# Optimization experiments

Measured on AMD Instinct MI355X. Metric: run time of the kernel, lower is better.

Reference implementation:

```python
import jax, jax.numpy as jnp
import numpy as np
import math

DIM = 2048
H = 16
KV = 4
HD = DIM // H  # 128
ROPE_DIM = 64  # head_dim * rope_fraction(0.5), even
ROPE_BASE = 10000.0
EPS_RMS = 1.1920928955078125e-07  # torch fp32 finfo eps (F.rms_norm default)


def rms_norm(t):
    # F.rms_norm over last dim, no weight
    return t * jax.lax.rsqrt(jnp.mean(t * t, axis=-1, keepdims=True) + EPS_RMS)


def rope_tables(seqlen, dtype):
    inv_freq = 1.0 / (ROPE_BASE ** (jnp.arange(0, ROPE_DIM, 2, dtype=jnp.float32) / ROPE_DIM))
    t = jnp.arange(seqlen, dtype=jnp.float32)
    freqs = jnp.outer(t, inv_freq)  # [S, ROPE_DIM//2]
    return jnp.cos(freqs).astype(dtype)[None, None], jnp.sin(freqs).astype(dtype)[None, None]


def apply_partial_rope(x, cos, sin):
    # x: [B, h, S, HD]; rotate first ROPE_DIM dims, pass through the rest
    xr = x[..., :ROPE_DIM]
    half = ROPE_DIM // 2
    x1, x2 = xr[..., :half], xr[..., half:]
    rotated = jnp.concatenate((x1 * cos + x2 * sin, -x1 * sin + x2 * cos), axis=-1)
    return jnp.concatenate((rotated, x[..., ROPE_DIM:]), axis=-1)


def setup_inputs() -> dict:
    key = jax.random.key(0)
    ks = jax.random.split(key, 5)
    B, S = 4, 1024
    x = jax.random.normal(ks[0], (B, S, DIM), dtype=jnp.float32)
    Wq = jax.random.normal(ks[1], (DIM, DIM), dtype=jnp.float32) * 0.02
    Wk = jax.random.normal(ks[2], (KV * HD, DIM), dtype=jnp.float32) * 0.02
    Wv = jax.random.normal(ks[3], (KV * HD, DIM), dtype=jnp.float32) * 0.02
    Wproj = jax.random.normal(ks[4], (DIM, DIM), dtype=jnp.float32) * 0.02
    # causal boolean mask [B, S, S]
    causal = jnp.tril(jnp.ones((S, S), dtype=bool))
    attn_mask = jnp.broadcast_to(causal[None], (B, S, S))
    return {"x": x, "attn_mask": attn_mask, "Wq": Wq, "Wk": Wk, "Wv": Wv, "Wproj": Wproj}


def reference(x, attn_mask, Wq, Wk, Wv, Wproj):
    B, S, D = x.shape
    repeat = H // KV
    q = (x @ Wq.T).reshape(B, S, H, HD).transpose(0, 2, 1, 3)   # [B,H,S,HD]
    k = (x @ Wk.T).reshape(B, S, KV, HD).transpose(0, 2, 1, 3)  # [B,KV,S,HD]
    v = (x @ Wv.T).reshape(B, S, KV, HD).transpose(0, 2, 1, 3)
    q = rms_norm(q)
    k = rms_norm(k)
    cos, sin = rope_tables(S, q.dtype)
    q = apply_partial_rope(q, cos, sin)
    k = apply_partial_rope(k, cos, sin)
    # GQA: expand kv heads
    k_rep = jnp.repeat(k, repeat, axis=1)  # [B,H,S,HD]
    v_rep = jnp.repeat(v, repeat, axis=1)
    bias = jnp.where(attn_mask[:, None], jnp.float32(0.0), jnp.float32(-10000.0)).astype(q.dtype)
    scores = jnp.einsum('bhqd,bhkd->bhqk', q, k_rep) / math.sqrt(HD) + bias
    attn = jax.nn.softmax(scores, axis=-1)
    y = jnp.einsum('bhqk,bhkd->bhqd', attn, v_rep)
    valid = jnp.any(attn_mask, axis=-1)[:, None, :, None].astype(y.dtype)
    y = y * valid
    # xsa: remove component of y along self value vector
    denom = jnp.maximum(jnp.sum(v_rep * v_rep, axis=-1, keepdims=True), 1e-06)
    proj = jnp.sum(y * v_rep, axis=-1, keepdims=True) / denom
    y = y - proj * v_rep
    y = y.transpose(0, 2, 1, 3).reshape(B, S, D)
    return y @ Wproj.T
```

## Files before the change

kernel.cpp:

```cpp
#include <hip/hip_runtime.h>


typedef __attribute__((ext_vector_type(8))) __bf16 bf16x8;
typedef __attribute__((ext_vector_type(4))) __bf16 bf16x4;
typedef __attribute__((ext_vector_type(4))) float f32x4;

static_assert(sizeof(__bf16) == 2, "bf16 size");

#define MFMA16x16x32(a, b, c) __builtin_amdgcn_mfma_f32_16x16x32_bf16((a), (b), (c), 0, 0, 0)

#if __has_builtin(__builtin_amdgcn_exp2f)
#define EXP2(x) __builtin_amdgcn_exp2f(x)
#else
#define EXP2(x) exp2f(x)
#endif

__device__ __forceinline__ void gload_lds16(const void* g, void* l) {
  __builtin_amdgcn_global_load_lds((const __attribute__((address_space(1))) void*)g,
                                   (__attribute__((address_space(3))) void*)l, 16, 0, 0);
}

__global__ __launch_bounds__(256) void prep(const float* __restrict__ x,
                                            const float* __restrict__ wq,
                                            const float* __restrict__ wk,
                                            const float* __restrict__ wv,
                                            const float* __restrict__ wp,
                                            __bf16* __restrict__ xb,
                                            __bf16* __restrict__ wb,
                                            __bf16* __restrict__ wpb,
                                            float2* __restrict__ tab) {
  constexpr int NX = 2097152;
  constexpr int NW1 = 1048576;
  constexpr int NW2 = 262144;
  constexpr int NP = 1048576;
  constexpr int NT = 32768;
  constexpr int TOT = NX + NW1 + 2 * NW2 + NP + NT;
  auto cast4 = [](const float* s, __bf16* d, int i) {
    f32x4 v = ((const f32x4*)s)[i];
    bf16x4 o;
    o[0] = (__bf16)v[0];
    o[1] = (__bf16)v[1];
    o[2] = (__bf16)v[2];
    o[3] = (__bf16)v[3];
    ((bf16x4*)d)[i] = o;
  };
  int i = blockIdx.x * blockDim.x + threadIdx.x;
  const int stride = gridDim.x * blockDim.x;
  for (; i < TOT; i += stride) {
    int j = i;
    if (j < NX) {
      cast4(x, xb, j);
    } else if ((j -= NX) < NW1) {
      cast4(wq, wb, j);
    } else if ((j -= NW1) < NW2) {
      cast4(wk, wb + (size_t)NW1 * 4, j);
    } else if ((j -= NW2) < NW2) {
      cast4(wv, wb + (size_t)(NW1 + NW2) * 4, j);
    } else if ((j -= NW2) < NP) {
      cast4(wp, wpb, j);
    } else {
      j -= NP;
      const int s = j >> 5, jj = j & 31;
      const float inv = powf(10000.0f, -(float)jj * 0.03125f);
      const float ang = (float)s * inv;
      tab[j] = make_float2(cosf(ang), sinf(ang));
    }
  }
}

template <typename CT, bool FUSE>
__global__ __launch_bounds__(256) void gemm_bt(const __bf16* __restrict__ A,
                                               const __bf16* __restrict__ B,
                                               CT* __restrict__ C, int N, int K, int nbn,
                                               const float2* __restrict__ tab) {
  __shared__ __bf16 As[3][128 * 32];
  __shared__ __bf16 Bs[3][128 * 32];
  const int nwg = gridDim.x;
  const int id = blockIdx.x;
  const int xid = (id & 7) * (nwg >> 3) + (id >> 3);
  const int bm = xid / nbn;
  const int bn = xid - bm * nbn;
  const int t = threadIdx.x;
  const int l = t & 63, w = t >> 6;
  const int wr = w >> 1, wc = w & 1;
  const int lr = l & 15, lk = l >> 4;
  const __bf16* Ab = A + (size_t)bm * 128 * K;
  const __bf16* Bb = B + (size_t)bn * 128 * K;
  const int srow = t >> 2;
  const int scol = ((t & 3) ^ ((srow >> 1) & 3)) << 3;
  f32x4 acc[4][4] = {};

  auto stage = [&](int kt, int buf) {
    const int k0 = kt << 5;
    gload_lds16(Ab + (size_t)srow * K + k0 + scol, &As[buf][t * 8]);
    gload_lds16(Ab + (size_t)(srow + 64) * K + k0 + scol, &As[buf][2048 + t * 8]);
    gload_lds16(Bb + (size_t)srow * K + k0 + scol, &Bs[buf][t * 8]);
    gload_lds16(Bb + (size_t)(srow + 64) * K + k0 + scol, &Bs[buf][2048 + t * 8]);
  };

  stage(0, 0);
  stage(1, 1);
  asm volatile("s_waitcnt vmcnt(4)" ::: "memory");
  __builtin_amdgcn_s_barrier();

  const int NT = K >> 5;
  int cur = 0;
  for (int kt = 0; kt < NT; ++kt) {
    if (kt + 2 < NT) {
      int c2 = cur + 2;
      if (c2 >= 3) c2 -= 3;
      stage(kt + 2, c2);
    }

    bf16x8 af[4], bfr[4];
#pragma unroll
    for (int m = 0; m < 4; ++m) {
      const int row = wr * 64 + m * 16 + lr;
      af[m] = *(const bf16x8*)&As[cur][row * 32 + ((lk ^ ((row >> 1) & 3)) << 3)];
    }
#pragma unroll
    for (int n = 0; n < 4; ++n) {
      const int row = wc * 64 + n * 16 + lr;
      bfr[n] = *(const bf16x8*)&Bs[cur][row * 32 + ((lk ^ ((row >> 1) & 3)) << 3)];
    }
#pragma unroll
    for (int m = 0; m < 4; ++m)
#pragma unroll
      for (int n = 0; n < 4; ++n) acc[m][n] = MFMA16x16x32(af[m], bfr[n], acc[m][n]);

    if (kt + 2 < NT)
      asm volatile("s_waitcnt vmcnt(4)" ::: "memory");
    else
      asm volatile("s_waitcnt vmcnt(0)" ::: "memory");
    __builtin_amdgcn_s_barrier();

    ++cur;
    if (cur == 3) cur = 0;
  }

  if constexpr (FUSE) {
    if (bn < 20) {
      __syncthreads();
      __shared__ float Ls[2][128];
      float ssp[4][4];
#pragma unroll
      for (int m = 0; m < 4; ++m)
#pragma unroll
        for (int i = 0; i < 4; ++i) {
          float s = 0.0f;
#pragma unroll
          for (int n = 0; n < 4; ++n) s += acc[m][n][i] * acc[m][n][i];
#pragma unroll
          for (int off = 1; off < 16; off <<= 1) s += __shfl_xor(s, off);
          ssp[m][i] = s;
        }
      if (lr == 0) {
#pragma unroll
        for (int m = 0; m < 4; ++m)
#pragma unroll
          for (int i = 0; i < 4; ++i)
            Ls[wc][wr * 64 + m * 16 + lk * 4 + i] = ssp[m][i];
      }
      __syncthreads();
      const bool isq = (bn < 16);
      const float qs = isq ? 0.1275174457f : 1.0f;
#pragma unroll
      for (int m = 0; m < 4; ++m) {
#pragma unroll
        for (int i = 0; i < 4; ++i) {
          const int rl = wr * 64 + m * 16 + lk * 4 + i;
          const int rg = bm * 128 + rl;
          const float sc =
              rsqrtf((Ls[0][rl] + Ls[1][rl]) * (1.0f / 128.0f) +
                     1.1920928955078125e-07f) *
              qs;
          CT* Cr = C + (size_t)rg * N + bn * 128;
          if (wc == 0) {
            const int s = rg & 1023;
#pragma unroll
            for (int n = 0; n < 2; ++n) {
              const int j = n * 16 + lr;
              const float2 cs = tab[s * 32 + j];
              const float x1 = acc[m][n][i], x2 = acc[m][n + 2][i];
              Cr[j] = (CT)((x1 * cs.x + x2 * cs.y) * sc);
              Cr[j + 32] = (CT)((-x1 * cs.y + x2 * cs.x) * sc);
            }
          } else {
#pragma unroll
            for (int n = 0; n < 4; ++n)
              Cr[64 + n * 16 + lr] = (CT)(acc[m][n][i] * sc);
          }
        }
      }
      return;
    }
  }

#pragma unroll
  for (int m = 0; m < 4; ++m) {
    const int row0 = bm * 128 + wr * 64 + m * 16 + lk * 4;
#pragma unroll
    for (int n = 0; n < 4; ++n) {
      const int col = bn * 128 + wc * 64 + n * 16 + lr;
#pragma unroll
      for (int i = 0; i < 4; ++i) C[(size_t)(row0 + i) * N + col] = (CT)acc[m][n][i];
    }
  }
}

__global__ __launch_bounds__(256) void vtrans(const __bf16* __restrict__ qkv,
                                              __bf16* __restrict__ vt) {
  __shared__ __bf16 L[64 * 128];
  const int tile = blockIdx.x;
  const int st = tile & 15, bk = tile >> 4;
  const int b = bk >> 2, kvh = bk & 3;
  const int t = threadIdx.x;
  const int s0 = st * 64;
  const __bf16* src = qkv + ((size_t)(b * 1024 + s0)) * 3072 + 2560 + kvh * 128;
#pragma unroll
  for (int r = 0; r < 4; ++r) {
    const int off = r * 2048 + t * 8;
    const int s = off >> 7, d = off & 127;
    bf16x8 v = *(const bf16x8*)(src + (size_t)s * 3072 + d);
    *(bf16x8*)&L[s * 128 + (d ^ ((s & 7) << 3) ^ (((s >> 3) & 7) << 3))] = v;
  }
  __syncthreads();
  __bf16* dst = vt + (size_t)bk * 128 * 1024;
#pragma unroll
  for (int r = 0; r < 4; ++r) {
    const int off = r * 2048 + t * 8;
    const int d = off >> 6, sc = off & 63;
    bf16x8 v;
#pragma unroll
    for (int j = 0; j < 8; ++j) {
      const int s = sc + j;
      v[j] = L[s * 128 + (d ^ ((s & 7) << 3) ^ (((s >> 3) & 7) << 3))];
    }
    *(bf16x8*)&dst[(size_t)d * 1024 + ((s0 + sc) ^ ((d & 7) << 3))] = v;
  }
}

__global__ __launch_bounds__(512) void attn_fwd(const __bf16* __restrict__ qkv,
                                                const __bf16* __restrict__ vt,
                                                __bf16* __restrict__ y) {
  const int id = blockIdx.x;
  const int g = (id & 7) | (((id >> 3) & 1) << 3);
  const int b = g >> 2, kvh = g & 3;
  const int hi = (id >> 4) & 3;
  const int pr = (id >> 6) & 3;
  const int h = kvh * 4 + hi;

  const int t = threadIdx.x;
  const int l = t & 63, w = t >> 6;
  const int lr = l & 15, lk = l >> 4;
  const int lr8 = lr & 7;

  __shared__ __bf16 Ks[2][64 * 128];
  __shared__ __bf16 Vs[2][128 * 64];
  __shared__ __bf16 Ps[8][16 * 64];

  const size_t rb = (size_t)b * 1024;
  const __bf16* Kg0 = qkv + rb * 3072 + 2048 + kvh * 128;
  const __bf16* Vtb = vt + (size_t)(b * 4 + kvh) * 128 * 1024;

  const int koff0 = t * 8;
  const int krow0 = koff0 >> 7;
  const int kcol0 = (koff0 & 127) ^ ((krow0 & 7) << 3);
  const int koff1 = 4096 + t * 8;
  const int krow1 = koff1 >> 7;
  const int kcol1 = (koff1 & 127) ^ ((krow1 & 7) << 3);
  const int voff0 = t * 8, voff1 = 4096 + t * 8;

#pragma unroll 1
  for (int pass = 0; pass < 2; ++pass) {
    const int qt = pass ? (7 - pr) : pr;
    const int q0 = qt << 7;

    bf16x8 aq[4];
    {
      const __bf16* qrow = qkv + (rb + q0 + w * 16 + lr) * 3072 + h * 128 + lk * 8;
#pragma unroll
      for (int kk = 0; kk < 4; ++kk) aq[kk] = *(const bf16x8*)(qrow + kk * 32);
    }

    float m_i[4], l_i[4];
    f32x4 o[8] = {};
#pragma unroll
    for (int i = 0; i < 4; ++i) {
      m_i[i] = -1e30f;
      l_i[i] = 0.0f;
    }

    const int rowg0 = q0 + w * 16 + lk * 4;
    const int wmin = q0 + w * 16;
    const int wmax = wmin + 15;
    const int nt = 2 * qt + 2;

    gload_lds16(Kg0 + (size_t)krow0 * 3072 + kcol0, &Ks[0][0] + koff0);
    gload_lds16(Kg0 + (size_t)krow1 * 3072 + kcol1, &Ks[0][0] + koff1);
    gload_lds16(Vtb + (size_t)(voff0 >> 6) * 1024 + (voff0 & 63), &Vs[0][0] + voff0);
    gload_lds16(Vtb + (size_t)(voff1 >> 6) * 1024 + (voff1 & 63), &Vs[0][0] + voff1);
    __syncthreads();

    for (int tt = 0; tt < nt; ++tt) {
      const int kv0 = tt * 64;
      const int cur = tt & 1;
      if (tt + 1 < nt) {
        const int nkv = kv0 + 64;
        const __bf16* Kg = Kg0 + (size_t)nkv * 3072;
        __bf16* kd = &Ks[cur ^ 1][0];
        __bf16* vd = &Vs[cur ^ 1][0];
        gload_lds16(Kg + (size_t)krow0 * 3072 + kcol0, kd + koff0);
        gload_lds16(Kg + (size_t)krow1 * 3072 + kcol1, kd + koff1);
        gload_lds16(Vtb + (size_t)(voff0 >> 6) * 1024 + nkv + (voff0 & 63), vd + voff0);
        gload_lds16(Vtb + (size_t)(voff1 >> 6) * 1024 + nkv + (voff1 & 63), vd + voff1);
      }

      if (kv0 <= wmax) {
        f32x4 sacc[4] = {};
        __builtin_amdgcn_s_setprio(1);
#pragma unroll
        for (int kk = 0; kk < 4; ++kk) {
#pragma unroll
          for (int n = 0; n < 4; ++n) {
            const bf16x8 bk = *(const bf16x8*)&Ks[cur][(n * 16 + lr) * 128 +
                                                      ((kk * 32 + lk * 8) ^ (lr8 << 3))];
            sacc[n] = MFMA16x16x32(aq[kk], bk, sacc[n]);
          }
        }
        __builtin_amdgcn_s_setprio(0);

        float pm[4];
#pragma unroll
        for (int i = 0; i < 4; ++i) pm[i] = -1e30f;
        if (kv0 + 63 > wmin) {
#pragma unroll
          for (int n = 0; n < 4; ++n) {
            const int colg = kv0 + n * 16 + lr;
#pragma unroll
            for (int i = 0; i < 4; ++i) {
              if (colg > rowg0 + i) sacc[n][i] = -1e30f;
              pm[i] = fmaxf(pm[i], sacc[n][i]);
            }
          }
        } else {
#pragma unroll
          for (int n = 0; n < 4; ++n)
#pragma unroll
            for (int i = 0; i < 4; ++i) pm[i] = fmaxf(pm[i], sacc[n][i]);
        }
#pragma unroll
        for (int i = 0; i < 4; ++i) {
          pm[i] = fmaxf(pm[i], __shfl_xor(pm[i], 1));
          pm[i] = fmaxf(pm[i], __shfl_xor(pm[i], 2));
          pm[i] = fmaxf(pm[i], __shfl_xor(pm[i], 4));
          pm[i] = fmaxf(pm[i], __shfl_xor(pm[i], 8));
        }
        float alpha[4], rs[4];
#pragma unroll
        for (int i = 0; i < 4; ++i) {
          const float mn = fmaxf(m_i[i], pm[i]);
          alpha[i] = EXP2(m_i[i] - mn);
          m_i[i] = mn;
          rs[i] = 0.0f;
        }
#pragma unroll
        for (int n = 0; n < 4; ++n) {
#pragma unroll
          for (int i = 0; i < 4; ++i) {
            const float p = EXP2(sacc[n][i] - m_i[i]);
            rs[i] += p;
            const int prow = lk * 4 + i;
            Ps[w][prow * 64 + ((n * 16 + lr) ^ ((prow & 7) << 3))] = (__bf16)p;
          }
        }
#pragma unroll
        for (int i = 0; i < 4; ++i) {
          rs[i] += __shfl_xor(rs[i], 1);
          rs[i] += __shfl_xor(rs[i], 2);
          rs[i] += __shfl_xor(rs[i], 4);
          rs[i] += __shfl_xor(rs[i], 8);
          l_i[i] = l_i[i] * alpha[i] + rs[i];
        }
#pragma unroll
        for (int f = 0; f < 8; ++f)
#pragma unroll
          for (int i = 0; i < 4; ++i) o[f][i] *= alpha[i];

        __builtin_amdgcn_s_setprio(1);
#pragma unroll
        for (int ks = 0; ks < 2; ++ks) {
          const bf16x8 pa =
              *(const bf16x8*)&Ps[w][lr * 64 + ((ks * 32 + lk * 8) ^ (lr8 << 3))];
#pragma unroll
          for (int f = 0; f < 8; ++f) {
            const bf16x8 vb = *(const bf16x8*)&Vs[cur][(f * 16 + lr) * 64 +
                                                       ((ks * 32 + lk * 8) ^ (lr8 << 3))];
            o[f] = MFMA16x16x32(pa, vb, o[f]);
          }
        }
        __builtin_amdgcn_s_setprio(0);
      }

      __syncthreads();
    }

#pragma unroll
    for (int i = 0; i < 4; ++i) {
      const int sg = rowg0 + i;
      const size_t mg = rb + sg;
      const __bf16* vp = qkv + mg * 3072 + 2560 + kvh * 128;
      const float invl = 1.0f / l_i[i];
      float vvv[8], yvv[8];
      float dyv = 0.0f, dvv = 0.0f;
#pragma unroll
      for (int f = 0; f < 8; ++f) {
        const float vf = (float)vp[f * 16 + lr];
        const float yf = o[f][i] * invl;
        vvv[f] = vf;
        yvv[f] = yf;
        dyv += yf * vf;
        dvv += vf * vf;
      }
#pragma unroll
      for (int off = 1; off < 16; off <<= 1) {
        dyv += __shfl_xor(dyv, off);
        dvv += __shfl_xor(dvv, off);
      }
      const float proj = dyv / fmaxf(dvv, 1e-6f);
      __bf16* yp = y + mg * 2048 + h * 128;
#pragma unroll
      for (int f = 0; f < 8; ++f) yp[f * 16 + lr] = (__bf16)(yvv[f] - proj * vvv[f]);
    }
  }
}

extern "C" void kernel_launch(void* const* d_in, const int* in_sizes, int n_in,
                              void* d_out, int out_size, void* d_ws, size_t ws_size,
                              hipStream_t stream) {
  const float* x = (const float*)d_in[0];
  const float* Wq = (const float*)d_in[2];
  const float* Wk = (const float*)d_in[3];
  const float* Wv = (const float*)d_in[4];
  const float* Wp = (const float*)d_in[5];
  float* out = (float*)d_out;

  __bf16* xb = (__bf16*)d_ws;
  __bf16* Wb = xb + (size_t)4096 * 2048;
  __bf16* Wpb = Wb + (size_t)3072 * 2048;
  __bf16* qkv = Wpb + (size_t)2048 * 2048;
  __bf16* yb = qkv + (size_t)4096 * 3072;
  float2* tab = (float2*)(yb + (size_t)4096 * 2048);
  __bf16* vt = xb;

  prep<<<2048, 256, 0, stream>>>(x, Wq, Wk, Wv, Wp, xb, Wb, Wpb, tab);

  gemm_bt<__bf16, true><<<768, 256, 0, stream>>>(xb, Wb, qkv, 3072, 2048, 24, tab);
  vtrans<<<256, 256, 0, stream>>>(qkv, vt);
  attn_fwd<<<256, 512, 0, stream>>>(qkv, vt, yb);
  gemm_bt<float, false><<<512, 256, 0, stream>>>(yb, Wpb, out, 2048, 2048, 16, nullptr);
}
```

Before: 183.6 us.

## Process both causal query tiles concurrently in one 1024-thread attention block

The attention kernel no longer runs two sequential passes over paired query tiles (pr and 7-pr). It launches 1024 threads, where waves 0-7 handle the long tile and waves 8-15 the short tile, and both share each K/V tile load. This halves K/V global traffic for the short tile and removes the second pass's pipeline restart. In exchange it raises register and LDS pressure per block, and the short-tile waves sit idle at barriers once their causal range ends.

```diff
diff --git a/kernel.cpp b/kernel.cpp
--- a/kernel.cpp
+++ b/kernel.cpp
@@ -240,9 +240,9 @@
   }
 }
 
-__global__ __launch_bounds__(512) void attn_fwd(const __bf16* __restrict__ qkv,
-                                                const __bf16* __restrict__ vt,
-                                                __bf16* __restrict__ y) {
+__global__ __launch_bounds__(1024) void attn_fwd(const __bf16* __restrict__ qkv,
+                                                 const __bf16* __restrict__ vt,
+                                                 __bf16* __restrict__ y) {
   const int id = blockIdx.x;
   const int g = (id & 7) | (((id >> 3) & 1) << 3);
   const int b = g >> 2, kvh = g & 3;
@@ -254,184 +254,173 @@
   const int l = t & 63, w = t >> 6;
   const int lr = l & 15, lk = l >> 4;
   const int lr8 = lr & 7;
+  const int w8 = w & 7;
 
   __shared__ __bf16 Ks[2][64 * 128];
   __shared__ __bf16 Vs[2][128 * 64];
-  __shared__ __bf16 Ps[8][16 * 64];
+  __shared__ __bf16 Ps[16][16 * 64];
 
   const size_t rb = (size_t)b * 1024;
   const __bf16* Kg0 = qkv + rb * 3072 + 2048 + kvh * 128;
   const __bf16* Vtb = vt + (size_t)(b * 4 + kvh) * 128 * 1024;
 
-  const int koff0 = t * 8;
-  const int krow0 = koff0 >> 7;
-  const int kcol0 = (koff0 & 127) ^ ((krow0 & 7) << 3);
-  const int koff1 = 4096 + t * 8;
-  const int krow1 = koff1 >> 7;
-  const int kcol1 = (koff1 & 127) ^ ((krow1 & 7) << 3);
-  const int voff0 = t * 8, voff1 = 4096 + t * 8;
-
-#pragma unroll 1
-  for (int pass = 0; pass < 2; ++pass) {
-    const int qt = pass ? (7 - pr) : pr;
-    const int q0 = qt << 7;
-
-    bf16x8 aq[4];
-    {
-      const __bf16* qrow = qkv + (rb + q0 + w * 16 + lr) * 3072 + h * 128 + lk * 8;
-#pragma unroll
-      for (int kk = 0; kk < 4; ++kk) aq[kk] = *(const bf16x8*)(qrow + kk * 32);
-    }
-
-    float m_i[4], l_i[4];
-    f32x4 o[8] = {};
-#pragma unroll
-    for (int i = 0; i < 4; ++i) {
-      m_i[i] = -1e30f;
-      l_i[i] = 0.0f;
-    }
-
-    const int rowg0 = q0 + w * 16 + lk * 4;
-    const int wmin = q0 + w * 16;
-    const int wmax = wmin + 15;
-    const int nt = 2 * qt + 2;
-
-    gload_lds16(Kg0 + (size_t)krow0 * 3072 + kcol0, &Ks[0][0] + koff0);
-    gload_lds16(Kg0 + (size_t)krow1 * 3072 + kcol1, &Ks[0][0] + koff1);
-    gload_lds16(Vtb + (size_t)(voff0 >> 6) * 1024 + (voff0 & 63), &Vs[0][0] + voff0);
-    gload_lds16(Vtb + (size_t)(voff1 >> 6) * 1024 + (voff1 & 63), &Vs[0][0] + voff1);
+  const int koff = t * 8;
+  const int krow = koff >> 7;
+  const int kcol = (koff & 127) ^ ((krow & 7) << 3);
+  const int voff = t * 8;
+
+  const int qt = (w < 8) ? (7 - pr) : pr;
+  const int q0 = qt << 7;
+
+  bf16x8 aq[4];
+  {
+    const __bf16* qrow = qkv + (rb + q0 + w8 * 16 + lr) * 3072 + h * 128 + lk * 8;
+#pragma unroll
+    for (int kk = 0; kk < 4; ++kk) aq[kk] = *(const bf16x8*)(qrow + kk * 32);
+  }
+
+  float m_i[4], l_i[4];
+  f32x4 o[8] = {};
+#pragma unroll
+  for (int i = 0; i < 4; ++i) {
+    m_i[i] = -1e30f;
+    l_i[i] = 0.0f;
+  }
+
+  const int rowg0 = q0 + w8 * 16 + lk * 4;
+  const int wmin = q0 + w8 * 16;
+  const int wmax = wmin + 15;
+  const int nt = 2 * (7 - pr) + 2;
+
+  gload_lds16(Kg0 + (size_t)krow * 3072 + kcol, &Ks[0][0] + koff);
+  gload_lds16(Vtb + (size_t)(voff >> 6) * 1024 + (voff & 63), &Vs[0][0] + voff);
+  __syncthreads();
+
+  for (int tt = 0; tt < nt; ++tt) {
+    const int kv0 = tt * 64;
+    const int cur = tt & 1;
+    if (tt + 1 < nt) {
+      const int nkv = kv0 + 64;
+      gload_lds16(Kg0 + (size_t)(nkv + krow) * 3072 + kcol, &Ks[cur ^ 1][0] + koff);
+      gload_lds16(Vtb + (size_t)(voff >> 6) * 1024 + nkv + (voff & 63),
+                  &Vs[cur ^ 1][0] + voff);
+    }
+
+    if (kv0 <= wmax) {
+      f32x4 sacc[4] = {};
+      __builtin_amdgcn_s_setprio(1);
+#pragma unroll
+      for (int kk = 0; kk < 4; ++kk) {
+#pragma unroll
+        for (int n = 0; n < 4; ++n) {
+          const bf16x8 bk = *(const bf16x8*)&Ks[cur][(n * 16 + lr) * 128 +
+                                                    ((kk * 32 + lk * 8) ^ (lr8 << 3))];
+          sacc[n] = MFMA16x16x32(aq[kk], bk, sacc[n]);
+        }
+      }
+      __builtin_amdgcn_s_setprio(0);
+
+      float pm[4];
+#pragma unroll
+      for (int i = 0; i < 4; ++i) pm[i] = -1e30f;
+      if (kv0 + 63 > wmin) {
+#pragma unroll
+        for (int n = 0; n < 4; ++n) {
+          const int colg = kv0 + n * 16 + lr;
+#pragma unroll
+          for (int i = 0; i < 4; ++i) {
+            if (colg > rowg0 + i) sacc[n][i] = -1e30f;
+            pm[i] = fmaxf(pm[i], sacc[n][i]);
+          }
+        }
+      } else {
+#pragma unroll
+        for (int n = 0; n < 4; ++n)
+#pragma unroll
+          for (int i = 0; i < 4; ++i) pm[i] = fmaxf(pm[i], sacc[n][i]);
+      }
+#pragma unroll
+      for (int i = 0; i < 4; ++i) {
+        pm[i] = fmaxf(pm[i], __shfl_xor(pm[i], 1));
+        pm[i] = fmaxf(pm[i], __shfl_xor(pm[i], 2));
+        pm[i] = fmaxf(pm[i], __shfl_xor(pm[i], 4));
+        pm[i] = fmaxf(pm[i], __shfl_xor(pm[i], 8));
+      }
+      float alpha[4], rs[4];
+#pragma unroll
+      for (int i = 0; i < 4; ++i) {
+        const float mn = fmaxf(m_i[i], pm[i]);
+        alpha[i] = EXP2(m_i[i] - mn);
+        m_i[i] = mn;
+        rs[i] = 0.0f;
+      }
+#pragma unroll
+      for (int n = 0; n < 4; ++n) {
+#pragma unroll
+        for (int i = 0; i < 4; ++i) {
+          const float p = EXP2(sacc[n][i] - m_i[i]);
+          rs[i] += p;
+          const int prow = lk * 4 + i;
+          Ps[w][prow * 64 + ((n * 16 + lr) ^ ((prow & 7) << 3))] = (__bf16)p;
+        }
+      }
+#pragma unroll
+      for (int i = 0; i < 4; ++i) {
+        rs[i] += __shfl_xor(rs[i], 1);
+        rs[i] += __shfl_xor(rs[i], 2);
+        rs[i] += __shfl_xor(rs[i], 4);
+        rs[i] += __shfl_xor(rs[i], 8);
+        l_i[i] = l_i[i] * alpha[i] + rs[i];
+      }
+#pragma unroll
+      for (int f = 0; f < 8; ++f)
+#pragma unroll
+        for (int i = 0; i < 4; ++i) o[f][i] *= alpha[i];
+
+      __builtin_amdgcn_s_setprio(1);
+#pragma unroll
+      for (int ks = 0; ks < 2; ++ks) {
+        const bf16x8 pa =
+            *(const bf16x8*)&Ps[w][lr * 64 + ((ks * 32 + lk * 8) ^ (lr8 << 3))];
+#pragma unroll
+        for (int f = 0; f < 8; ++f) {
+          const bf16x8 vb = *(const bf16x8*)&Vs[cur][(f * 16 + lr) * 64 +
+                                                     ((ks * 32 + lk * 8) ^ (lr8 << 3))];
+          o[f] = MFMA16x16x32(pa, vb, o[f]);
+        }
+      }
+      __builtin_amdgcn_s_setprio(0);
+    }
+
     __syncthreads();
-
-    for (int tt = 0; tt < nt; ++tt) {
-      const int kv0 = tt * 64;
-      const int cur = tt & 1;
-      if (tt + 1 < nt) {
-        const int nkv = kv0 + 64;
-        const __bf16* Kg = Kg0 + (size_t)nkv * 3072;
-        __bf16* kd = &Ks[cur ^ 1][0];
-        __bf16* vd = &Vs[cur ^ 1][0];
-        gload_lds16(Kg + (size_t)krow0 * 3072 + kcol0, kd + koff0);
-        gload_lds16(Kg + (size_t)krow1 * 3072 + kcol1, kd + koff1);
-        gload_lds16(Vtb + (size_t)(voff0 >> 6) * 1024 + nkv + (voff0 & 63), vd + voff0);
-        gload_lds16(Vtb + (size_t)(voff1 >> 6) * 1024 + nkv + (voff1 & 63), vd + voff1);
-      }
-
-      if (kv0 <= wmax) {
-        f32x4 sacc[4] = {};
-        __builtin_amdgcn_s_setprio(1);
-#pragma unroll
-        for (int kk = 0; kk < 4; ++kk) {
-#pragma unroll
-          for (int n = 0; n < 4; ++n) {
-            const bf16x8 bk = *(const bf16x8*)&Ks[cur][(n * 16 + lr) * 128 +
-                                                      ((kk * 32 + lk * 8) ^ (lr8 << 3))];
-            sacc[n] = MFMA16x16x32(aq[kk], bk, sacc[n]);
-          }
-        }
-        __builtin_amdgcn_s_setprio(0);
-
-        float pm[4];
-#pragma unroll
-        for (int i = 0; i < 4; ++i) pm[i] = -1e30f;
-        if (kv0 + 63 > wmin) {
-#pragma unroll
-          for (int n = 0; n < 4; ++n) {
-            const int colg = kv0 + n * 16 + lr;
-#pragma unroll
-            for (int i = 0; i < 4; ++i) {
-              if (colg > rowg0 + i) sacc[n][i] = -1e30f;
-              pm[i] = fmaxf(pm[i], sacc[n][i]);
-            }
-          }
-        } else {
-#pragma unroll
-          for (int n = 0; n < 4; ++n)
-#pragma unroll
-            for (int i = 0; i < 4; ++i) pm[i] = fmaxf(pm[i], sacc[n][i]);
-        }
-#pragma unroll
-        for (int i = 0; i < 4; ++i) {
-          pm[i] = fmaxf(pm[i], __shfl_xor(pm[i], 1));
-          pm[i] = fmaxf(pm[i], __shfl_xor(pm[i], 2));
-          pm[i] = fmaxf(pm[i], __shfl_xor(pm[i], 4));
-          pm[i] = fmaxf(pm[i], __shfl_xor(pm[i], 8));
-        }
-        float alpha[4], rs[4];
-#pragma unroll
-        for (int i = 0; i < 4; ++i) {
-          const float mn = fmaxf(m_i[i], pm[i]);
-          alpha[i] = EXP2(m_i[i] - mn);
-          m_i[i] = mn;
-          rs[i] = 0.0f;
-        }
-#pragma unroll
-        for (int n = 0; n < 4; ++n) {
-#pragma unroll
-          for (int i = 0; i < 4; ++i) {
-            const float p = EXP2(sacc[n][i] - m_i[i]);
-            rs[i] += p;
-            const int prow = lk * 4 + i;
-            Ps[w][prow * 64 + ((n * 16 + lr) ^ ((prow & 7) << 3))] = (__bf16)p;
-          }
-        }
-#pragma unroll
-        for (int i = 0; i < 4; ++i) {
-          rs[i] += __shfl_xor(rs[i], 1);
-          rs[i] += __shfl_xor(rs[i], 2);
-          rs[i] += __shfl_xor(rs[i], 4);
-          rs[i] += __shfl_xor(rs[i], 8);
-          l_i[i] = l_i[i] * alpha[i] + rs[i];
-        }
-#pragma unroll
-        for (int f = 0; f < 8; ++f)
-#pragma unroll
-          for (int i = 0; i < 4; ++i) o[f][i] *= alpha[i];
-
-        __builtin_amdgcn_s_setprio(1);
-#pragma unroll
-        for (int ks = 0; ks < 2; ++ks) {
-          const bf16x8 pa =
-              *(const bf16x8*)&Ps[w][lr * 64 + ((ks * 32 + lk * 8) ^ (lr8 << 3))];
-#pragma unroll
-          for (int f = 0; f < 8; ++f) {
-            const bf16x8 vb = *(const bf16x8*)&Vs[cur][(f * 16 + lr) * 64 +
-                                                       ((ks * 32 + lk * 8) ^ (lr8 << 3))];
-            o[f] = MFMA16x16x32(pa, vb, o[f]);
-          }
-        }
-        __builtin_amdgcn_s_setprio(0);
-      }
-
-      __syncthreads();
-    }
-
-#pragma unroll
-    for (int i = 0; i < 4; ++i) {
-      const int sg = rowg0 + i;
-      const size_t mg = rb + sg;
-      const __bf16* vp = qkv + mg * 3072 + 2560 + kvh * 128;
-      const float invl = 1.0f / l_i[i];
-      float vvv[8], yvv[8];
-      float dyv = 0.0f, dvv = 0.0f;
-#pragma unroll
-      for (int f = 0; f < 8; ++f) {
-        const float vf = (float)vp[f * 16 + lr];
-        const float yf = o[f][i] * invl;
-        vvv[f] = vf;
-        yvv[f] = yf;
-        dyv += yf * vf;
-        dvv += vf * vf;
-      }
-#pragma unroll
-      for (int off = 1; off < 16; off <<= 1) {
-        dyv += __shfl_xor(dyv, off);
-        dvv += __shfl_xor(dvv, off);
-      }
-      const float proj = dyv / fmaxf(dvv, 1e-6f);
-      __bf16* yp = y + mg * 2048 + h * 128;
-#pragma unroll
-      for (int f = 0; f < 8; ++f) yp[f * 16 + lr] = (__bf16)(yvv[f] - proj * vvv[f]);
-    }
+  }
+
+#pragma unroll
+  for (int i = 0; i < 4; ++i) {
+    const int sg = rowg0 + i;
+    const size_t mg = rb + sg;
+    const __bf16* vp = qkv + mg * 3072 + 2560 + kvh * 128;
+    const float invl = 1.0f / l_i[i];
+    float vvv[8], yvv[8];
+    float dyv = 0.0f, dvv = 0.0f;
+#pragma unroll
+    for (int f = 0; f < 8; ++f) {
+      const float vf = (float)vp[f * 16 + lr];
+      const float yf = o[f][i] * invl;
+      vvv[f] = vf;
+      yvv[f] = yf;
+      dyv += yf * vf;
+      dvv += vf * vf;
+    }
+#pragma unroll
+    for (int off = 1; off < 16; off <<= 1) {
+      dyv += __shfl_xor(dyv, off);
+      dvv += __shfl_xor(dvv, off);
+    }
+    const float proj = dyv / fmaxf(dvv, 1e-6f);
+    __bf16* yp = y + mg * 2048 + h * 128;
+#pragma unroll
+    for (int f = 0; f < 8; ++f) yp[f * 16 + lr] = (__bf16)(yvv[f] - proj * vvv[f]);
   }
 }
 
@@ -457,6 +446,6 @@
 
   gemm_bt<__bf16, true><<<768, 256, 0, stream>>>(xb, Wb, qkv, 3072, 2048, 24, tab);
   vtrans<<<256, 256, 0, stream>>>(qkv, vt);
-  attn_fwd<<<256, 512, 0, stream>>>(qkv, vt, yb);
+  attn_fwd<<<256, 1024, 0, stream>>>(qkv, vt, yb);
   gemm_bt<float, false><<<512, 256, 0, stream>>>(yb, Wpb, out, 2048, 2048, 16, nullptr);
 }
```

Measured after the change: 183.0 us. About the same (-0.3%).

## Use 128-wide KV tiles in attention and swap pass order to process long tiles first

Applied to the files above, without the earlier changes.

The attention kernel's KV tile grows from 64 to 128 keys. That halves the number of loop iterations, barriers and online-softmax rescales per query tile, and the per-wave causal skip is dropped because tiles now line up with the 128-row query tile. Shared memory roughly doubles (K, V and P buffers), which can lower occupancy, and waves on the diagonal tile now compute fully masked sub-blocks. The two passes also swap order so the longer query tile runs first, for better tail balance.

```diff
diff --git a/kernel.cpp b/kernel.cpp
--- a/kernel.cpp
+++ b/kernel.cpp
@@ -255,26 +255,36 @@
   const int lr = l & 15, lk = l >> 4;
   const int lr8 = lr & 7;
 
-  __shared__ __bf16 Ks[2][64 * 128];
-  __shared__ __bf16 Vs[2][128 * 64];
-  __shared__ __bf16 Ps[8][16 * 64];
+  __shared__ __bf16 Ks[2][128 * 128];
+  __shared__ __bf16 Vs[2][128 * 128];
+  __shared__ __bf16 Ps[8][16 * 128];
 
   const size_t rb = (size_t)b * 1024;
   const __bf16* Kg0 = qkv + rb * 3072 + 2048 + kvh * 128;
   const __bf16* Vtb = vt + (size_t)(b * 4 + kvh) * 128 * 1024;
 
-  const int koff0 = t * 8;
-  const int krow0 = koff0 >> 7;
-  const int kcol0 = (koff0 & 127) ^ ((krow0 & 7) << 3);
-  const int koff1 = 4096 + t * 8;
-  const int krow1 = koff1 >> 7;
-  const int kcol1 = (koff1 & 127) ^ ((krow1 & 7) << 3);
-  const int voff0 = t * 8, voff1 = 4096 + t * 8;
+  const int srow = t >> 4;
+  const int scg = t & 15;
+  const int kcolg = (scg ^ (srow & 7)) << 3;
+
+  auto stageK = [&](int kv0, int buf) {
+#pragma unroll
+    for (int r = 0; r < 4; ++r)
+      gload_lds16(Kg0 + (size_t)(kv0 + r * 32 + srow) * 3072 + kcolg,
+                  &Ks[buf][0] + r * 4096 + t * 8);
+  };
+  auto stageV = [&](int kv0, int buf) {
+#pragma unroll
+    for (int r = 0; r < 4; ++r)
+      gload_lds16(Vtb + (size_t)(r * 32 + srow) * 1024 + kv0 + scg * 8,
+                  &Vs[buf][0] + r * 4096 + t * 8);
+  };
 
 #pragma unroll 1
   for (int pass = 0; pass < 2; ++pass) {
-    const int qt = pass ? (7 - pr) : pr;
+    const int qt = pass ? pr : (7 - pr);
     const int q0 = qt << 7;
+    const int nt = qt + 1;
 
     bf16x8 aq[4];
     {
@@ -292,115 +302,102 @@
     }
 
     const int rowg0 = q0 + w * 16 + lk * 4;
-    const int wmin = q0 + w * 16;
-    const int wmax = wmin + 15;
-    const int nt = 2 * qt + 2;
-
-    gload_lds16(Kg0 + (size_t)krow0 * 3072 + kcol0, &Ks[0][0] + koff0);
-    gload_lds16(Kg0 + (size_t)krow1 * 3072 + kcol1, &Ks[0][0] + koff1);
-    gload_lds16(Vtb + (size_t)(voff0 >> 6) * 1024 + (voff0 & 63), &Vs[0][0] + voff0);
-    gload_lds16(Vtb + (size_t)(voff1 >> 6) * 1024 + (voff1 & 63), &Vs[0][0] + voff1);
+
+    stageK(0, 0);
+    stageV(0, 0);
     __syncthreads();
 
     for (int tt = 0; tt < nt; ++tt) {
-      const int kv0 = tt * 64;
+      const int kv0 = tt << 7;
       const int cur = tt & 1;
       if (tt + 1 < nt) {
-        const int nkv = kv0 + 64;
-        const __bf16* Kg = Kg0 + (size_t)nkv * 3072;
-        __bf16* kd = &Ks[cur ^ 1][0];
-        __bf16* vd = &Vs[cur ^ 1][0];
-        gload_lds16(Kg + (size_t)krow0 * 3072 + kcol0, kd + koff0);
-        gload_lds16(Kg + (size_t)krow1 * 3072 + kcol1, kd + koff1);
-        gload_lds16(Vtb + (size_t)(voff0 >> 6) * 1024 + nkv + (voff0 & 63), vd + voff0);
-        gload_lds16(Vtb + (size_t)(voff1 >> 6) * 1024 + nkv + (voff1 & 63), vd + voff1);
-      }
-
-      if (kv0 <= wmax) {
-        f32x4 sacc[4] = {};
-        __builtin_amdgcn_s_setprio(1);
-#pragma unroll
-        for (int kk = 0; kk < 4; ++kk) {
-#pragma unroll
-          for (int n = 0; n < 4; ++n) {
-            const bf16x8 bk = *(const bf16x8*)&Ks[cur][(n * 16 + lr) * 128 +
-                                                      ((kk * 32 + lk * 8) ^ (lr8 << 3))];
-            sacc[n] = MFMA16x16x32(aq[kk], bk, sacc[n]);
+        stageK(kv0 + 128, cur ^ 1);
+        stageV(kv0 + 128, cur ^ 1);
+      }
+
+      f32x4 sacc[8] = {};
+      __builtin_amdgcn_s_setprio(1);
+#pragma unroll
+      for (int kk = 0; kk < 4; ++kk) {
+#pragma unroll
+        for (int n = 0; n < 8; ++n) {
+          const bf16x8 bk = *(const bf16x8*)&Ks[cur][(n * 16 + lr) * 128 +
+                                                    ((kk * 32 + lk * 8) ^ (lr8 << 3))];
+          sacc[n] = MFMA16x16x32(aq[kk], bk, sacc[n]);
+        }
+      }
+      __builtin_amdgcn_s_setprio(0);
+
+      float pm[4];
+#pragma unroll
+      for (int i = 0; i < 4; ++i) pm[i] = -1e30f;
+      if (tt == qt) {
+#pragma unroll
+        for (int n = 0; n < 8; ++n) {
+          const int colg = kv0 + n * 16 + lr;
+#pragma unroll
+          for (int i = 0; i < 4; ++i) {
+            if (colg > rowg0 + i) sacc[n][i] = -1e30f;
+            pm[i] = fmaxf(pm[i], sacc[n][i]);
           }
         }
-        __builtin_amdgcn_s_setprio(0);
-
-        float pm[4];
-#pragma unroll
-        for (int i = 0; i < 4; ++i) pm[i] = -1e30f;
-        if (kv0 + 63 > wmin) {
-#pragma unroll
-          for (int n = 0; n < 4; ++n) {
-            const int colg = kv0 + n * 16 + lr;
-#pragma unroll
-            for (int i = 0; i < 4; ++i) {
-              if (colg > rowg0 + i) sacc[n][i] = -1e30f;
-              pm[i] = fmaxf(pm[i], sacc[n][i]);
-            }
-          }
-        } else {
-#pragma unroll
-          for (int n = 0; n < 4; ++n)
-#pragma unroll
-            for (int i = 0; i < 4; ++i) pm[i] = fmaxf(pm[i], sacc[n][i]);
-        }
+      } else {
+#pragma unroll
+        for (int n = 0; n < 8; ++n)
+#pragma unroll
+          for (int i = 0; i < 4; ++i) pm[i] = fmaxf(pm[i], sacc[n][i]);
+      }
+#pragma unroll
+      for (int i = 0; i < 4; ++i) {
+        pm[i] = fmaxf(pm[i], __shfl_xor(pm[i], 1));
+        pm[i] = fmaxf(pm[i], __shfl_xor(pm[i], 2));
+        pm[i] = fmaxf(pm[i], __shfl_xor(pm[i], 4));
+        pm[i] = fmaxf(pm[i], __shfl_xor(pm[i], 8));
+      }
+      float alpha[4], rs[4];
+#pragma unroll
+      for (int i = 0; i < 4; ++i) {
+        const float mn = fmaxf(m_i[i], pm[i]);
+        alpha[i] = EXP2(m_i[i] - mn);
+        m_i[i] = mn;
+        rs[i] = 0.0f;
+      }
+#pragma unroll
+      for (int n = 0; n < 8; ++n) {
 #pragma unroll
         for (int i = 0; i < 4; ++i) {
-          pm[i] = fmaxf(pm[i], __shfl_xor(pm[i], 1));
-          pm[i] = fmaxf(pm[i], __shfl_xor(pm[i], 2));
-          pm[i] = fmaxf(pm[i], __shfl_xor(pm[i], 4));
-          pm[i] = fmaxf(pm[i], __shfl_xor(pm[i], 8));
-        }
-        float alpha[4], rs[4];
-#pragma unroll
-        for (int i = 0; i < 4; ++i) {
-          const float mn = fmaxf(m_i[i], pm[i]);
-          alpha[i] = EXP2(m_i[i] - mn);
-          m_i[i] = mn;
-          rs[i] = 0.0f;
-        }
-#pragma unroll
-        for (int n = 0; n < 4; ++n) {
-#pragma unroll
-          for (int i = 0; i < 4; ++i) {
-            const float p = EXP2(sacc[n][i] - m_i[i]);
-            rs[i] += p;
-            const int prow = lk * 4 + i;
-            Ps[w][prow * 64 + ((n * 16 + lr) ^ ((prow & 7) << 3))] = (__bf16)p;
-          }
-        }
-#pragma unroll
-        for (int i = 0; i < 4; ++i) {
-          rs[i] += __shfl_xor(rs[i], 1);
-          rs[i] += __shfl_xor(rs[i], 2);
-          rs[i] += __shfl_xor(rs[i], 4);
-          rs[i] += __shfl_xor(rs[i], 8);
-          l_i[i] = l_i[i] * alpha[i] + rs[i];
-        }
-#pragma unroll
-        for (int f = 0; f < 8; ++f)
-#pragma unroll
-          for (int i = 0; i < 4; ++i) o[f][i] *= alpha[i];
-
-        __builtin_amdgcn_s_setprio(1);
-#pragma unroll
-        for (int ks = 0; ks < 2; ++ks) {
-          const bf16x8 pa =
-              *(const bf16x8*)&Ps[w][lr * 64 + ((ks * 32 + lk * 8) ^ (lr8 << 3))];
-#pragma unroll
-          for (int f = 0; f < 8; ++f) {
-            const bf16x8 vb = *(const bf16x8*)&Vs[cur][(f * 16 + lr) * 64 +
-                                                       ((ks * 32 + lk * 8) ^ (lr8 << 3))];
-            o[f] = MFMA16x16x32(pa, vb, o[f]);
-          }
-        }
-        __builtin_amdgcn_s_setprio(0);
-      }
+          const float p = EXP2(sacc[n][i] - m_i[i]);
+          rs[i] += p;
+          const int prow = lk * 4 + i;
+          Ps[w][prow * 128 + ((n * 16 + lr) ^ ((prow & 7) << 3))] = (__bf16)p;
+        }
+      }
+#pragma unroll
+      for (int i = 0; i < 4; ++i) {
+        rs[i] += __shfl_xor(rs[i], 1);
+        rs[i] += __shfl_xor(rs[i], 2);
+        rs[i] += __shfl_xor(rs[i], 4);
+        rs[i] += __shfl_xor(rs[i], 8);
+        l_i[i] = l_i[i] * alpha[i] + rs[i];
+      }
+#pragma unroll
+      for (int f = 0; f < 8; ++f)
+#pragma unroll
+        for (int i = 0; i < 4; ++i) o[f][i] *= alpha[i];
+
+      __builtin_amdgcn_s_setprio(1);
+#pragma unroll
+      for (int ks = 0; ks < 4; ++ks) {
+        const bf16x8 pa =
+            *(const bf16x8*)&Ps[w][lr * 128 + ((ks * 32 + lk * 8) ^ (lr8 << 3))];
+#pragma unroll
+        for (int f = 0; f < 8; ++f) {
+          const bf16x8 vb = *(const bf16x8*)&Vs[cur][(f * 16 + lr) * 128 +
+                                                     ((ks * 32 + lk * 8) ^ (lr8 << 3))];
+          o[f] = MFMA16x16x32(pa, vb, o[f]);
+        }
+      }
+      __builtin_amdgcn_s_setprio(0);
 
       __syncthreads();
     }
```

New measurement: 178.7 us. -2.6%, faster.
